# Optimization experiments

Hardware: AMD Instinct MI355X
Metric: run time of the kernel (lower is better)

The kernel has to match this reference:

```python
import jax, jax.numpy as jnp
import numpy as np

IN_FEATURES = 4096
OUT_FEATURES = 11008
BLOCK_SIZE = 64
BITS = 4
RANGE_MAX = 2 ** (BITS - 1) - 1  # 7


def setup_inputs() -> dict:
    key = jax.random.key(0)
    k1, k2, k3, k4 = jax.random.split(key, 4)
    n_blocks = OUT_FEATURES * IN_FEATURES // BLOCK_SIZE
    x = jax.random.normal(k1, (4, 2048, IN_FEATURES), dtype=jnp.float32)
    # int4 codes in [-7, 7]; stored signed int. Use randint in [-7, 8).
    weight_quant = jax.random.randint(k2, (n_blocks, BLOCK_SIZE), -RANGE_MAX, RANGE_MAX + 1, dtype=jnp.int32)
    weight_absmax = jax.random.uniform(k3, (n_blocks, 1), dtype=jnp.float32, minval=1e-5, maxval=1.0)
    bias = jax.random.normal(k4, (OUT_FEATURES,), dtype=jnp.float32)
    return {"x": x, "weight_quant": weight_quant, "weight_absmax": weight_absmax, "bias": bias}


def reference(x, weight_quant, weight_absmax, bias):
    # Blockwise dequant: q/range_max * absmax per block, reshape to (out, in). padding=0.
    w = (weight_quant.astype(jnp.float32) / RANGE_MAX) * weight_absmax  # [n_blocks, block]
    w = w.reshape(OUT_FEATURES, IN_FEATURES)
    # F.linear: y = x @ W^T + b
    return jnp.einsum('bsi,oi->bso', x, w) + bias
```

## Files before the change

### kernel.cpp

```cpp
#include <hip/hip_runtime.h>


#define K_DIM 4096
#define N_DIM 11008
#define M_DIM 8192
#define NT_K 64

typedef _Float16 f16;
typedef _Float16 f16x8 __attribute__((ext_vector_type(8)));
typedef float f32x4 __attribute__((ext_vector_type(4)));

__device__ __forceinline__ void gload16(const void* g, void* lds) {
  __builtin_amdgcn_global_load_lds(
      (__attribute__((address_space(1))) void*)g,
      (__attribute__((address_space(3))) void*)lds,
      16, 0, 0);
}

__global__ __launch_bounds__(256) void cvt_x_kernel(const float* __restrict__ x,
                                                    f16* __restrict__ xo, int n8) {
  int i = blockIdx.x * blockDim.x + threadIdx.x;
  if (i >= n8) return;
  const float4* xv = (const float4*)x;
  float4 a = xv[2 * i];
  float4 b = xv[2 * i + 1];
  f16x8 o;
  o[0] = (f16)a.x; o[1] = (f16)a.y; o[2] = (f16)a.z; o[3] = (f16)a.w;
  o[4] = (f16)b.x; o[5] = (f16)b.y; o[6] = (f16)b.z; o[7] = (f16)b.w;
  *(f16x8*)(xo + (size_t)i * 8) = o;
}

__global__ __launch_bounds__(256) void dequant_kernel(const int* __restrict__ q,
                                                      const float* __restrict__ amax,
                                                      f16* __restrict__ wo, int n8) {
  int i = blockIdx.x * blockDim.x + threadIdx.x;
  if (i >= n8) return;
  const int4* qv = (const int4*)q;
  int4 a = qv[2 * i];
  int4 b = qv[2 * i + 1];
  float s = amax[i >> 3] * (1.0f / 7.0f);
  f16x8 o;
  o[0] = (f16)((float)a.x * s); o[1] = (f16)((float)a.y * s);
  o[2] = (f16)((float)a.z * s); o[3] = (f16)((float)a.w * s);
  o[4] = (f16)((float)b.x * s); o[5] = (f16)((float)b.y * s);
  o[6] = (f16)((float)b.z * s); o[7] = (f16)((float)b.w * s);
  *(f16x8*)(wo + (size_t)i * 8) = o;
}

__global__ __launch_bounds__(512, 2) void gemm_f16_bt(const f16* __restrict__ A,
                                                      const f16* __restrict__ B,
                                                      const float* __restrict__ bias,
                                                      float* __restrict__ C) {
  __shared__ __align__(16) char lds[131072];

  const int tid = threadIdx.x;
  const int w = tid >> 6;
  const int l = tid & 63;
  const int wr = w >> 2;
  const int wc = w & 3;

  const int wg = blockIdx.x;
  const int swz = (wg & 7) * 172 + (wg >> 3);
  const int mt = swz / 43;
  const int nt = swz % 43;
  const int m0 = mt * 256;
  const int n0 = nt * 256;

  const int lr = l & 15;
  const int g = l >> 4;
  const int laneoff = ((lr >> 1) << 7) | (((((lr & 1) << 6) | (g << 4))) ^ (((lr >> 1) & 7) << 4));

  const char* Asrc[2];
  const char* Bsrc[2];
#pragma unroll
  for (int j = 0; j < 2; ++j) {
    const int u = ((j * 8 + w) << 10) + l * 16;
    const int r = u >> 7;
    const int cp = (u & 127) ^ ((r & 7) << 4);
    const int ra = 2 * r + (cp >> 6);
    const int kb = cp & 63;
    Asrc[j] = (const char*)A + (size_t)(m0 + ra) * (K_DIM * 2) + kb;
    Bsrc[j] = (const char*)B + (size_t)(n0 + ra) * (K_DIM * 2) + kb;
  }

  char* ldsc = (char*)lds;

#define STAGE_A(dst_off, koff)                              \
  {                                                         \
    char* d_ = ldsc + (dst_off) + w * 1024;                 \
    gload16(Asrc[0] + (koff), d_);                          \
    gload16(Asrc[1] + (koff), d_ + 8192);                   \
  }
#define STAGE_B(dst_off, koff)                              \
  {                                                         \
    char* d_ = ldsc + (dst_off) + w * 1024;                 \
    gload16(Bsrc[0] + (koff), d_);                          \
    gload16(Bsrc[1] + (koff), d_ + 8192);                   \
  }

  f32x4 acc[8][4];
#pragma unroll
  for (int i = 0; i < 8; ++i)
#pragma unroll
    for (int j = 0; j < 4; ++j) acc[i][j] = (f32x4){0.f, 0.f, 0.f, 0.f};

  STAGE_B(65536, 0);
  STAGE_A(0, 0);
  STAGE_B(65536 + 16384, 64);
  STAGE_A(16384, 64);
  STAGE_B(65536 + 32768, 128);
  STAGE_A(32768, 128);
  STAGE_B(65536 + 32768 + 16384, 192);
  asm volatile("s_waitcnt vmcnt(10)" ::: "memory");
  __builtin_amdgcn_s_barrier();

  for (int t = 0; t < NT_K; ++t) {
    const int p = t & 1;
    const int pn = p ^ 1;
    const int Ab = p * 32768;
    const int Bb = 65536 + p * 32768;
    const int t1 = (t + 1 < NT_K) ? (t + 1) : (NT_K - 1);
    const int t2 = (t + 2 < NT_K) ? (t + 2) : (NT_K - 1);
    const int k1 = t1 * 128;
    const int k2 = t2 * 128;

    f16x8 bf[4];
    f16x8 af[4];
#pragma unroll
    for (int pi = 0; pi < 4; ++pi) {
      const int kk = pi >> 1;
      const int mh = pi & 1;

      if (mh == 0) {
#pragma unroll
        for (int ni = 0; ni < 4; ++ni)
          bf[ni] = *(const f16x8*)(ldsc + Bb + kk * 16384 + ((wc * 64 + ni * 16) << 6) + laneoff);
      }
#pragma unroll
      for (int mi = 0; mi < 4; ++mi)
        af[mi] = *(const f16x8*)(ldsc + Ab + kk * 16384 +
                                 ((wr * 128 + mh * 64 + mi * 16) << 6) + laneoff);

      if (pi == 0) {
        STAGE_A(pn * 32768 + 16384, k1 + 64);
      } else if (pi == 1) {
        STAGE_B(65536 + p * 32768, k2);
      } else if (pi == 2) {
        STAGE_A(p * 32768, k2);
      } else {
        STAGE_B(65536 + p * 32768 + 16384, k2 + 64);
      }

      __builtin_amdgcn_s_barrier();
      __builtin_amdgcn_s_setprio(1);
#pragma unroll
      for (int mi = 0; mi < 4; ++mi)
#pragma unroll
        for (int ni = 0; ni < 4; ++ni)
          acc[mh * 4 + mi][ni] = __builtin_amdgcn_mfma_f32_16x16x32_f16(
              af[mi], bf[ni], acc[mh * 4 + mi][ni], 0, 0, 0);
      __builtin_amdgcn_s_setprio(0);
      if (mh == 1) asm volatile("s_waitcnt vmcnt(10)" ::: "memory");
      __builtin_amdgcn_s_barrier();
    }
  }

  const int orow = g * 4;
  float bv[4];
#pragma unroll
  for (int ni = 0; ni < 4; ++ni) bv[ni] = bias[n0 + wc * 64 + ni * 16 + lr];
#pragma unroll
  for (int mi = 0; mi < 8; ++mi) {
    const int row = m0 + wr * 128 + mi * 16 + orow;
#pragma unroll
    for (int ni = 0; ni < 4; ++ni) {
      const size_t cb = (size_t)row * N_DIM + (n0 + wc * 64 + ni * 16 + lr);
#pragma unroll
      for (int j = 0; j < 4; ++j) C[cb + (size_t)j * N_DIM] = acc[mi][ni][j] + bv[ni];
    }
  }
#undef STAGE_A
#undef STAGE_B
}

extern "C" void kernel_launch(void* const* d_in, const int* in_sizes, int n_in,
                              void* d_out, int out_size, void* d_ws, size_t ws_size,
                              hipStream_t stream) {
  const float* x = (const float*)d_in[0];
  const int* wq = (const int*)d_in[1];
  const float* amax = (const float*)d_in[2];
  const float* bias = (const float*)d_in[3];
  float* out = (float*)d_out;

  f16* Xh = (f16*)d_ws;
  f16* Wh = (f16*)((char*)d_ws + (size_t)M_DIM * K_DIM * 2);

  {
    int n8 = M_DIM * K_DIM / 8;
    cvt_x_kernel<<<n8 / 256, 256, 0, stream>>>(x, Xh, n8);
  }
  {
    int n8 = N_DIM * K_DIM / 8;
    dequant_kernel<<<n8 / 256, 256, 0, stream>>>(wq, amax, Wh, n8);
  }
  {
    dim3 grid((M_DIM / 256) * (N_DIM / 256));
    gemm_f16_bt<<<grid, 512, 0, stream>>>(Xh, Wh, bias, out);
  }
}
```

Before: 820.1 us.

## Triple-buffer A tiles in LDS, fuse prep kernels, use nontemporal memory ops

The GEMM now keeps three rotating A buffers in LDS (160KB total) instead of two. A loads are issued two k-steps ahead, with the staging order and vmcnt waits adjusted to match, so more global-to-LDS traffic can overlap with MFMA work. The fp32-to-fp16 conversion of x and the weight dequant are merged into one launch. That launch uses nontemporal loads, and the GEMM writes its output with nontemporal stores. The risks are using the full LDS capacity and the chance that the changed wait counts do not cover the new ordering of in-flight loads.

```diff
diff --git a/kernel.cpp b/kernel.cpp
--- a/kernel.cpp
+++ b/kernel.cpp
@@ -5,10 +5,13 @@
 #define N_DIM 11008
 #define M_DIM 8192
 #define NT_K 64
+#define AB_OFF 98304
 
 typedef _Float16 f16;
 typedef _Float16 f16x8 __attribute__((ext_vector_type(8)));
 typedef float f32x4 __attribute__((ext_vector_type(4)));
+typedef float fv4 __attribute__((ext_vector_type(4)));
+typedef int iv4 __attribute__((ext_vector_type(4)));
 
 __device__ __forceinline__ void gload16(const void* g, void* lds) {
   __builtin_amdgcn_global_load_lds(
@@ -17,41 +20,41 @@
       16, 0, 0);
 }
 
-__global__ __launch_bounds__(256) void cvt_x_kernel(const float* __restrict__ x,
-                                                    f16* __restrict__ xo, int n8) {
+__global__ __launch_bounds__(256) void prep_kernel(const float* __restrict__ x,
+                                                   f16* __restrict__ xo, int n8x,
+                                                   const int* __restrict__ q,
+                                                   const float* __restrict__ amax,
+                                                   f16* __restrict__ wo, int n8w) {
   int i = blockIdx.x * blockDim.x + threadIdx.x;
-  if (i >= n8) return;
-  const float4* xv = (const float4*)x;
-  float4 a = xv[2 * i];
-  float4 b = xv[2 * i + 1];
-  f16x8 o;
-  o[0] = (f16)a.x; o[1] = (f16)a.y; o[2] = (f16)a.z; o[3] = (f16)a.w;
-  o[4] = (f16)b.x; o[5] = (f16)b.y; o[6] = (f16)b.z; o[7] = (f16)b.w;
-  *(f16x8*)(xo + (size_t)i * 8) = o;
-}
-
-__global__ __launch_bounds__(256) void dequant_kernel(const int* __restrict__ q,
-                                                      const float* __restrict__ amax,
-                                                      f16* __restrict__ wo, int n8) {
-  int i = blockIdx.x * blockDim.x + threadIdx.x;
-  if (i >= n8) return;
-  const int4* qv = (const int4*)q;
-  int4 a = qv[2 * i];
-  int4 b = qv[2 * i + 1];
-  float s = amax[i >> 3] * (1.0f / 7.0f);
-  f16x8 o;
-  o[0] = (f16)((float)a.x * s); o[1] = (f16)((float)a.y * s);
-  o[2] = (f16)((float)a.z * s); o[3] = (f16)((float)a.w * s);
-  o[4] = (f16)((float)b.x * s); o[5] = (f16)((float)b.y * s);
-  o[6] = (f16)((float)b.z * s); o[7] = (f16)((float)b.w * s);
-  *(f16x8*)(wo + (size_t)i * 8) = o;
+  if (i < n8x) {
+    const fv4* xv = (const fv4*)x;
+    fv4 a = __builtin_nontemporal_load(xv + 2 * (size_t)i);
+    fv4 b = __builtin_nontemporal_load(xv + 2 * (size_t)i + 1);
+    f16x8 o;
+    o[0] = (f16)a.x; o[1] = (f16)a.y; o[2] = (f16)a.z; o[3] = (f16)a.w;
+    o[4] = (f16)b.x; o[5] = (f16)b.y; o[6] = (f16)b.z; o[7] = (f16)b.w;
+    *(f16x8*)(xo + (size_t)i * 8) = o;
+  } else {
+    int j = i - n8x;
+    if (j >= n8w) return;
+    const iv4* qv = (const iv4*)q;
+    iv4 a = __builtin_nontemporal_load(qv + 2 * (size_t)j);
+    iv4 b = __builtin_nontemporal_load(qv + 2 * (size_t)j + 1);
+    float s = amax[j >> 3] * (1.0f / 7.0f);
+    f16x8 o;
+    o[0] = (f16)((float)a.x * s); o[1] = (f16)((float)a.y * s);
+    o[2] = (f16)((float)a.z * s); o[3] = (f16)((float)a.w * s);
+    o[4] = (f16)((float)b.x * s); o[5] = (f16)((float)b.y * s);
+    o[6] = (f16)((float)b.z * s); o[7] = (f16)((float)b.w * s);
+    *(f16x8*)(wo + (size_t)j * 8) = o;
+  }
 }
 
 __global__ __launch_bounds__(512, 2) void gemm_f16_bt(const f16* __restrict__ A,
                                                       const f16* __restrict__ B,
                                                       const float* __restrict__ bias,
                                                       float* __restrict__ C) {
-  __shared__ __align__(16) char lds[131072];
+  __shared__ __align__(16) char lds[163840];
 
   const int tid = threadIdx.x;
   const int w = tid >> 6;
@@ -85,17 +88,17 @@
 
   char* ldsc = (char*)lds;
 
-#define STAGE_A(dst_off, koff)                              \
-  {                                                         \
-    char* d_ = ldsc + (dst_off) + w * 1024;                 \
-    gload16(Asrc[0] + (koff), d_);                          \
-    gload16(Asrc[1] + (koff), d_ + 8192);                   \
-  }
-#define STAGE_B(dst_off, koff)                              \
-  {                                                         \
-    char* d_ = ldsc + (dst_off) + w * 1024;                 \
-    gload16(Bsrc[0] + (koff), d_);                          \
-    gload16(Bsrc[1] + (koff), d_ + 8192);                   \
+#define STAGE_A(dst_off, koff)              \
+  {                                         \
+    char* d_ = ldsc + (dst_off) + w * 1024; \
+    gload16(Asrc[0] + (koff), d_);          \
+    gload16(Asrc[1] + (koff), d_ + 8192);   \
+  }
+#define STAGE_B(dst_off, koff)              \
+  {                                         \
+    char* d_ = ldsc + (dst_off) + w * 1024; \
+    gload16(Bsrc[0] + (koff), d_);          \
+    gload16(Bsrc[1] + (koff), d_ + 8192);   \
   }
 
   f32x4 acc[8][4];
@@ -104,24 +107,24 @@
 #pragma unroll
     for (int j = 0; j < 4; ++j) acc[i][j] = (f32x4){0.f, 0.f, 0.f, 0.f};
 
-  STAGE_B(65536, 0);
   STAGE_A(0, 0);
-  STAGE_B(65536 + 16384, 64);
   STAGE_A(16384, 64);
-  STAGE_B(65536 + 32768, 128);
+  STAGE_B(AB_OFF, 0);
+  STAGE_B(AB_OFF + 16384, 64);
   STAGE_A(32768, 128);
-  STAGE_B(65536 + 32768 + 16384, 192);
-  asm volatile("s_waitcnt vmcnt(10)" ::: "memory");
+  STAGE_A(32768 + 16384, 192);
+  STAGE_B(AB_OFF + 32768, 128);
+  STAGE_B(AB_OFF + 32768 + 16384, 192);
+  asm volatile("s_waitcnt vmcnt(8)" ::: "memory");
   __builtin_amdgcn_s_barrier();
+
+  int ap = 0;
+  int ap2 = 65536;
 
   for (int t = 0; t < NT_K; ++t) {
     const int p = t & 1;
-    const int pn = p ^ 1;
-    const int Ab = p * 32768;
-    const int Bb = 65536 + p * 32768;
-    const int t1 = (t + 1 < NT_K) ? (t + 1) : (NT_K - 1);
+    const int Bb = AB_OFF + p * 32768;
     const int t2 = (t + 2 < NT_K) ? (t + 2) : (NT_K - 1);
-    const int k1 = t1 * 128;
     const int k2 = t2 * 128;
 
     f16x8 bf[4];
@@ -138,17 +141,17 @@
       }
 #pragma unroll
       for (int mi = 0; mi < 4; ++mi)
-        af[mi] = *(const f16x8*)(ldsc + Ab + kk * 16384 +
+        af[mi] = *(const f16x8*)(ldsc + ap + kk * 16384 +
                                  ((wr * 128 + mh * 64 + mi * 16) << 6) + laneoff);
 
       if (pi == 0) {
-        STAGE_A(pn * 32768 + 16384, k1 + 64);
+        STAGE_A(ap2, k2);
       } else if (pi == 1) {
-        STAGE_B(65536 + p * 32768, k2);
+        STAGE_A(ap2 + 16384, k2 + 64);
       } else if (pi == 2) {
-        STAGE_A(p * 32768, k2);
+        STAGE_B(Bb, k2);
       } else {
-        STAGE_B(65536 + p * 32768 + 16384, k2 + 64);
+        STAGE_B(Bb + 16384, k2 + 64);
       }
 
       __builtin_amdgcn_s_barrier();
@@ -160,9 +163,12 @@
           acc[mh * 4 + mi][ni] = __builtin_amdgcn_mfma_f32_16x16x32_f16(
               af[mi], bf[ni], acc[mh * 4 + mi][ni], 0, 0, 0);
       __builtin_amdgcn_s_setprio(0);
-      if (mh == 1) asm volatile("s_waitcnt vmcnt(10)" ::: "memory");
+      if (pi == 3) asm volatile("s_waitcnt vmcnt(8)" ::: "memory");
       __builtin_amdgcn_s_barrier();
     }
+
+    ap += 32768;  if (ap == AB_OFF) ap = 0;
+    ap2 += 32768; if (ap2 == AB_OFF) ap2 = 0;
   }
 
   const int orow = g * 4;
@@ -176,7 +182,8 @@
     for (int ni = 0; ni < 4; ++ni) {
       const size_t cb = (size_t)row * N_DIM + (n0 + wc * 64 + ni * 16 + lr);
 #pragma unroll
-      for (int j = 0; j < 4; ++j) C[cb + (size_t)j * N_DIM] = acc[mi][ni][j] + bv[ni];
+      for (int j = 0; j < 4; ++j)
+        __builtin_nontemporal_store(acc[mi][ni][j] + bv[ni], &C[cb + (size_t)j * N_DIM]);
     }
   }
 #undef STAGE_A
@@ -196,12 +203,10 @@
   f16* Wh = (f16*)((char*)d_ws + (size_t)M_DIM * K_DIM * 2);
 
   {
-    int n8 = M_DIM * K_DIM / 8;
-    cvt_x_kernel<<<n8 / 256, 256, 0, stream>>>(x, Xh, n8);
-  }
-  {
-    int n8 = N_DIM * K_DIM / 8;
-    dequant_kernel<<<n8 / 256, 256, 0, stream>>>(wq, amax, Wh, n8);
+    int n8x = M_DIM * K_DIM / 8;
+    int n8w = N_DIM * K_DIM / 8;
+    int nthr = n8x + n8w;
+    prep_kernel<<<(nthr + 255) / 256, 256, 0, stream>>>(x, Xh, n8x, wq, amax, Wh, n8w);
   }
   {
     dim3 grid((M_DIM / 256) * (N_DIM / 256));
```

New measurement: 769.2 us. 1.07x faster.
